# Optimization experiments

Hardware: AMD Instinct MI355X
Metric: run time of the kernel (lower is better)

## Reference

```python
import jax, jax.numpy as jnp
import numpy as np

N_NODES = 50000
N_EDGES = 1600000
POS_DIM = 64
IN_FEATS = 128
OUT_FEATS = 128
EDGE_MLP_DIM = 32


def setup_inputs() -> dict:
    key = jax.random.key(0)
    ks = jax.random.split(key, 8)
    x = jax.random.normal(ks[0], (N_NODES, POS_DIM + IN_FEATS), dtype=jnp.float32)
    edge_index = jax.random.randint(ks[1], (2, N_EDGES), 0, N_NODES, dtype=jnp.int32)
    # glorot for weight_noformer [in_feats, out_feats]
    stdv = float(np.sqrt(6.0 / (IN_FEATS + OUT_FEATS)))
    w_no = jax.random.uniform(ks[2], (IN_FEATS, OUT_FEATS), dtype=jnp.float32, minval=-stdv, maxval=stdv)
    bias = jnp.zeros((OUT_FEATS,), dtype=jnp.float32)
    # edge MLP: Linear(1, 32) -> Linear(32, 1) -> Sigmoid (no inner activation, faithful to source)
    lim1 = float(np.sqrt(1.0 / 1.0))
    mlp_w1 = jax.random.uniform(ks[3], (1, EDGE_MLP_DIM), dtype=jnp.float32, minval=-lim1, maxval=lim1)
    mlp_b1 = jax.random.uniform(ks[4], (EDGE_MLP_DIM,), dtype=jnp.float32, minval=-lim1, maxval=lim1)
    lim2 = float(np.sqrt(1.0 / EDGE_MLP_DIM))
    mlp_w2 = jax.random.uniform(ks[5], (EDGE_MLP_DIM, 1), dtype=jnp.float32, minval=-lim2, maxval=lim2)
    mlp_b2 = jax.random.uniform(ks[6], (1,), dtype=jnp.float32, minval=-lim2, maxval=lim2)
    return {"x": x, "edge_index": edge_index, "w_no": w_no, "bias": bias,
            "mlp_w1": mlp_w1, "mlp_b1": mlp_b1, "mlp_w2": mlp_w2, "mlp_b2": mlp_b2}


def reference(x, edge_index, w_no, bias, mlp_w1, mlp_b1, mlp_w2, mlp_b2):
    N = x.shape[0]
    coors = x[:, :POS_DIM]            # [N, pos_dim]
    feats = x[:, POS_DIM:]            # [N, in_feats]

    # gcn_norm with added self-loops (improved=False -> fill value 1)
    loop = jnp.arange(N, dtype=edge_index.dtype)
    row = jnp.concatenate([edge_index[0], loop])   # source
    col = jnp.concatenate([edge_index[1], loop])   # target
    ew = jnp.ones(row.shape[0], dtype=x.dtype)
    deg = jax.ops.segment_sum(ew, col, num_segments=N)
    dinv = jnp.where(deg > 0, jax.lax.rsqrt(deg), 0.0)
    ew = dinv[row] * ew * dinv[col]                # [E+N]

    # per-edge squared relative distance in positional space
    rel = coors[row] - coors[col]                  # [E+N, pos_dim]
    rel_dist = jnp.sum(rel * rel, axis=-1, keepdims=True)  # [E+N, 1]

    # tiny edge MLP + sigmoid (Linear -> Linear -> sigmoid)
    h = rel_dist @ mlp_w1 + mlp_b1                 # [E+N, mlp_dim]
    pe = jax.nn.sigmoid(h @ mlp_w2 + mlp_b2)       # [E+N, 1]

    # message = pe * norm_weight * x_j ; scatter-add into target nodes
    msg = pe * ew[:, None] * feats[row]            # [E+N, in_feats]
    m_i = jax.ops.segment_sum(msg, col, num_segments=N)  # [N, in_feats]

    hidden = m_i @ w_no + bias                     # [N, out_feats]
    return jnp.concatenate([coors, hidden], axis=-1)
```

## Files before the change

### kernel.cpp

```cpp
#include <hip/hip_runtime.h>
#include <math.h>

constexpr int NN = 50000;
constexpr int NE = 1600000;
constexpr int PD = 64;
constexpr int XD = 192;

constexpr int NB   = 3125;
constexpr int CAPF = 768;
constexpr int NCB  = 196;
constexpr int CAPC = 10240;
constexpr int RBLK = 782;
constexpr int CH2  = 5;

constexpr int OFF_NSQ   = 64;
constexpr int OFF_DINV  = OFF_NSQ   + 50048;
constexpr int OFF_HPRE  = OFF_DINV  + 50048;
constexpr int OFF_CCUR  = OFF_HPRE  + 50048;
constexpr int OFF_FCUR  = OFF_CCUR  + 256;
constexpr int OFF_CDATA = OFF_FCUR  + 3136;
constexpr int OFF_BDATA = OFF_CDATA + NCB * CAPC;
constexpr int OFF_CBQ   = OFF_BDATA + NB * CAPF;
constexpr int OFF_FBQ   = OFF_CBQ   + NN * 16;
constexpr int OFF_WBT   = OFF_FBQ   + NN * 32;

typedef __attribute__((ext_vector_type(8))) short bf16x8;
typedef __attribute__((ext_vector_type(4))) float f32x4;
typedef __attribute__((ext_vector_type(2))) float f32x2;

__device__ __forceinline__ unsigned short f2bf(float f) {
    unsigned u = __float_as_uint(f);
    return (unsigned short)((u + 0x7FFFu + ((u >> 16) & 1u)) >> 16);
}

__global__ __launch_bounds__(256) void k_pack(const float* __restrict__ x,
                                              const int* __restrict__ rowv,
                                              const int* __restrict__ colv,
                                              const float* __restrict__ w_no,
                                              const float* __restrict__ w1,
                                              const float* __restrict__ b1,
                                              const float* __restrict__ w2,
                                              const float* __restrict__ b2,
                                              float* __restrict__ out,
                                              unsigned* __restrict__ cbq,
                                              unsigned* __restrict__ fbqu,
                                              unsigned* __restrict__ ccur,
                                              unsigned* __restrict__ cdata,
                                              unsigned short* __restrict__ wbt,
                                              float* __restrict__ nsq,
                                              float* __restrict__ AB) {
    __shared__ int hist[NCB];
    __shared__ int pre[NCB];
    __shared__ unsigned gbase[NCB];
    __shared__ int scanbuf[256];
    __shared__ unsigned stag[2048];
    __shared__ unsigned char binof[2048];

    int t = threadIdx.x;
    if (blockIdx.x < RBLK) {
        int base = blockIdx.x * 2048;
        int cnt = NE - base; if (cnt > 2048) cnt = 2048;
        for (int i = t; i < NCB; i += 256) hist[i] = 0;
        __syncthreads();
        unsigned myrec[8]; int mybin[8], myrank[8];
        #pragma unroll
        for (int j = 0; j < 8; ++j) {
            int idx = base + j * 256 + t;
            mybin[j] = -1;
            if (idx < NE) {
                int c = colv[idx], r = rowv[idx];
                int bin = c >> 8;
                mybin[j]  = bin;
                myrank[j] = atomicAdd(&hist[bin], 1);
                myrec[j]  = ((unsigned)c << 16) | (unsigned)r;
            }
        }
        __syncthreads();
        int v = (t < NCB) ? hist[t] : 0;
        scanbuf[t] = v; __syncthreads();
        for (int d = 1; d < 256; d <<= 1) {
            int u = (t >= d) ? scanbuf[t - d] : 0;
            __syncthreads(); scanbuf[t] += u; __syncthreads();
        }
        if (t < NCB) {
            pre[t]   = scanbuf[t] - v;
            gbase[t] = v ? atomicAdd(&ccur[t], (unsigned)v) : 0u;
        }
        __syncthreads();
        #pragma unroll
        for (int j = 0; j < 8; ++j) {
            if (mybin[j] >= 0) {
                int slot = pre[mybin[j]] + myrank[j];
                stag[slot]  = myrec[j];
                binof[slot] = (unsigned char)mybin[j];
            }
        }
        __syncthreads();
        for (int s = t; s < cnt; s += 256) {
            int bin = binof[s];
            unsigned dst = gbase[bin] + (unsigned)(s - pre[bin]);
            if (dst < CAPC)
                cdata[(size_t)bin * CAPC + dst] = stag[s];
        }
        return;
    }

    int tid = (blockIdx.x - RBLK) * 256 + t;
    if (tid < 16384) wbt[tid] = f2bf(w_no[(tid & 127) * 128 + (tid >> 7)]);
    if (tid == 0) {
        float a = 0.f, b = 0.f;
        for (int k = 0; k < 32; ++k) { a += w1[k] * w2[k]; b += b1[k] * w2[k]; }
        AB[0] = a; AB[1] = b + b2[0];
    }
    int wid = tid >> 6, lane = tid & 63;
    if (wid < NN && lane < 48) {
        const float4 v = *(const float4*)&x[(size_t)wid * XD + lane * 4];
        if (lane < 16) {
            *(float4*)&out[(size_t)wid * XD + lane * 4] = v;
            unsigned p = 0;
            p = __builtin_amdgcn_cvt_pk_fp8_f32(v.x, v.y, p, false);
            p = __builtin_amdgcn_cvt_pk_fp8_f32(v.z, v.w, p, true);
            cbq[(size_t)wid * 16 + lane] = p;
            f32x2 lo = __builtin_amdgcn_cvt_pk_f32_fp8(p, false);
            f32x2 hi = __builtin_amdgcn_cvt_pk_f32_fp8(p, true);
            float ssq = lo.x * lo.x + lo.y * lo.y + hi.x * hi.x + hi.y * hi.y;
            #pragma unroll
            for (int o = 8; o >= 1; o >>= 1) ssq += __shfl_xor(ssq, o);
            if (lane == 0) nsq[wid] = ssq;
        } else {
            unsigned p = 0;
            p = __builtin_amdgcn_cvt_pk_fp8_f32(v.x, v.y, p, false);
            p = __builtin_amdgcn_cvt_pk_fp8_f32(v.z, v.w, p, true);
            fbqu[(size_t)wid * 32 + (lane - 16)] = p;
        }
    }
}

__global__ __launch_bounds__(256) void k_scat2(const unsigned* __restrict__ ccur,
                                               const unsigned* __restrict__ cdata,
                                               unsigned* __restrict__ fcur,
                                               unsigned* __restrict__ bdata) {
    __shared__ int hist[16];
    __shared__ int pre[16];
    __shared__ unsigned gbase[16];
    __shared__ unsigned stag[2048];
    __shared__ unsigned char binof[2048];

    int cb = blockIdx.x / CH2, k = blockIdx.x % CH2;
    int len = (int)ccur[cb]; if (len > CAPC) len = CAPC;
    int base = k * 2048;
    if (base >= len) return;
    int cnt = len - base; if (cnt > 2048) cnt = 2048;
    int t = threadIdx.x;
    if (t < 16) hist[t] = 0;
    __syncthreads();

    const unsigned* seg = cdata + (size_t)cb * CAPC + base;
    unsigned myrec[8]; int mybin[8], myrank[8];
    #pragma unroll
    for (int j = 0; j < 8; ++j) {
        int idx = j * 256 + t;
        mybin[j] = -1;
        if (idx < cnt) {
            unsigned rec = seg[idx];
            int c = (int)(rec >> 16);
            int bin = (c >> 4) & 15;
            mybin[j]  = bin;
            myrank[j] = atomicAdd(&hist[bin], 1);
            myrec[j]  = ((unsigned)(c & 15) << 16) | (rec & 0xFFFFu);
        }
    }
    __syncthreads();
    if (t == 0) {
        int run = 0;
        for (int i = 0; i < 16; ++i) { pre[i] = run; run += hist[i]; }
    }
    __syncthreads();
    if (t < 16)
        gbase[t] = hist[t] ? atomicAdd(&fcur[cb * 16 + t], (unsigned)hist[t]) : 0u;
    __syncthreads();
    #pragma unroll
    for (int j = 0; j < 8; ++j) {
        if (mybin[j] >= 0) {
            int slot = pre[mybin[j]] + myrank[j];
            stag[slot]  = myrec[j];
            binof[slot] = (unsigned char)mybin[j];
        }
    }
    __syncthreads();
    for (int s = t; s < cnt; s += 256) {
        int bin = binof[s];
        unsigned dst = gbase[bin] + (unsigned)(s - pre[bin]);
        if (dst < CAPF)
            bdata[(size_t)(cb * 16 + bin) * CAPF + dst] = stag[s];
    }
}

__global__ __launch_bounds__(256) void k_deg(const unsigned* __restrict__ fcur,
                                             const unsigned* __restrict__ bdata,
                                             unsigned* __restrict__ fbqu,
                                             float* __restrict__ dinv,
                                             unsigned* __restrict__ hpre) {
    __shared__ int hist[16];
    __shared__ int pre[16];
    __shared__ float sdv[16];
    int b = blockIdx.x, t = threadIdx.x;
    if (t < 16) hist[t] = 0;
    __syncthreads();

    int cnt = (int)fcur[b]; if (cnt > CAPF) cnt = CAPF;
    const unsigned* seg = bdata + (size_t)b * CAPF;
    for (int g = t; g < cnt; g += 256)
        atomicAdd(&hist[seg[g] >> 16], 1);
    __syncthreads();
    if (t == 0) {
        int run = 0;
        for (int i = 0; i < 16; ++i) { pre[i] = run; run += hist[i]; }
    }
    __syncthreads();
    if (t < 16) {
        int d = b * 16 + t;
        float dv = rsqrtf((float)hist[t] + 1.0f);
        sdv[t] = dv;
        dinv[d] = dv;
        hpre[d] = ((unsigned)pre[t] << 16) | (unsigned)hist[t];
    }
    __syncthreads();
    for (int i = t; i < 512; i += 256) {
        int d5 = i >> 5, q = i & 31;
        size_t idx = (size_t)(b * 16 + d5) * 32 + q;
        unsigned u = fbqu[idx];
        float dv = sdv[d5];
        f32x2 dv2 = {dv, dv};
        f32x2 lo = dv2 * __builtin_amdgcn_cvt_pk_f32_fp8(u, false);
        f32x2 hi = dv2 * __builtin_amdgcn_cvt_pk_f32_fp8(u, true);
        unsigned p = 0;
        p = __builtin_amdgcn_cvt_pk_fp8_f32(lo.x, lo.y, p, false);
        p = __builtin_amdgcn_cvt_pk_fp8_f32(hi.x, hi.y, p, true);
        fbqu[idx] = p;
    }
}

__global__ __launch_bounds__(256) void k_gather(const unsigned* __restrict__ fcur,
                                                const unsigned* __restrict__ bdata,
                                                const unsigned* __restrict__ cbq,
                                                const unsigned char* __restrict__ fbq,
                                                const float* __restrict__ nsq,
                                                const float* __restrict__ dinv,
                                                const unsigned* __restrict__ hpre,
                                                const float* __restrict__ AB,
                                                const float* __restrict__ bias,
                                                const unsigned short* __restrict__ wbt,
                                                float* __restrict__ out) {
    __shared__ unsigned srcL[CAPF + 64];
    __shared__ float    wgtL[CAPF + 64];
    __shared__ uint4    dcq[16][4];
    __shared__ unsigned mLu[16][68];
    __shared__ int preS[16];
    __shared__ int degS[16];
    __shared__ int curL[16];
    __shared__ float dvd[16];
    __shared__ float nsd[16];

    int b = blockIdx.x, t = threadIdx.x;

    if (t < 16) {
        int d = b * 16 + t;
        unsigned hp = hpre[d];
        preS[t] = (int)(hp >> 16);
        degS[t] = (int)(hp & 0xFFFFu);
        curL[t] = (int)(hp >> 16);
        dvd[t] = dinv[d];
        nsd[t] = nsq[d];
    }
    if (t < 64)
        dcq[t >> 2][t & 3] = ((const uint4*)(cbq + (size_t)(b * 16 + (t >> 2)) * 16))[t & 3];
    __syncthreads();

    float A = AB[0], Bc = AB[1];
    float sigB = __builtin_amdgcn_rcpf(1.0f + __expf(-Bc));

    int group = t >> 2, sub = t & 3;
    int cnt = (int)fcur[b]; if (cnt > CAPF) cnt = CAPF;
    const unsigned* seg = bdata + (size_t)b * CAPF;
    for (int base = 0; base < cnt; base += 64) {
        int g = base + group;
        bool valid = g < cnt;
        int gc = valid ? g : cnt - 1;
        unsigned rec = seg[gc];
        int d5 = rec >> 16;
        int s  = rec & 0xFFFF;
        float ns = nsq[s];
        uint4 sq = ((const uint4*)(cbq + (size_t)s * 16))[sub];
        uint4 dq = dcq[d5][sub];
        f32x2 dots = {0.f, 0.f};
        dots += __builtin_amdgcn_cvt_pk_f32_fp8(sq.x, false) *
                __builtin_amdgcn_cvt_pk_f32_fp8(dq.x, false);
        dots += __builtin_amdgcn_cvt_pk_f32_fp8(sq.x, true) *
                __builtin_amdgcn_cvt_pk_f32_fp8(dq.x, true);
        dots += __builtin_amdgcn_cvt_pk_f32_fp8(sq.y, false) *
                __builtin_amdgcn_cvt_pk_f32_fp8(dq.y, false);
        dots += __builtin_amdgcn_cvt_pk_f32_fp8(sq.y, true) *
                __builtin_amdgcn_cvt_pk_f32_fp8(dq.y, true);
        dots += __builtin_amdgcn_cvt_pk_f32_fp8(sq.z, false) *
                __builtin_amdgcn_cvt_pk_f32_fp8(dq.z, false);
        dots += __builtin_amdgcn_cvt_pk_f32_fp8(sq.z, true) *
                __builtin_amdgcn_cvt_pk_f32_fp8(dq.z, true);
        dots += __builtin_amdgcn_cvt_pk_f32_fp8(sq.w, false) *
                __builtin_amdgcn_cvt_pk_f32_fp8(dq.w, false);
        dots += __builtin_amdgcn_cvt_pk_f32_fp8(sq.w, true) *
                __builtin_amdgcn_cvt_pk_f32_fp8(dq.w, true);
        float sp = dots.x + dots.y;
        sp += __shfl_xor(sp, 1);
        sp += __shfl_xor(sp, 2);
        float ss = ns + nsd[d5] - 2.0f * sp;
        float w  = dvd[d5] *
                   __builtin_amdgcn_rcpf(1.0f + __expf(-(A * ss + Bc)));
        if (valid && sub == 0) {
            int slot = atomicAdd(&curL[d5], 1);
            srcL[slot] = (unsigned)s;
            wgtL[slot] = w;
        }
    }
    __syncthreads();

    int wl = t >> 6, lane = t & 63;
    int eslot = lane >> 4, dg = lane & 15;

    for (int i = 0; i < 4; ++i) {
        int d5 = wl * 4 + i;
        int d  = b * 16 + d5;

        int deg = degS[d5], s0 = preS[d5];
        float dv = dvd[d5];
        float w0 = (eslot == 0) ? dv * sigB : 0.f;
        f32x2 w02 = {w0, w0};
        uint2 fd = *(const uint2*)(fbq + (size_t)d * 128 + dg * 8);
        f32x2 a01 = w02 * __builtin_amdgcn_cvt_pk_f32_fp8(fd.x, false);
        f32x2 a23 = w02 * __builtin_amdgcn_cvt_pk_f32_fp8(fd.x, true);
        f32x2 a45 = w02 * __builtin_amdgcn_cvt_pk_f32_fp8(fd.y, false);
        f32x2 a67 = w02 * __builtin_amdgcn_cvt_pk_f32_fp8(fd.y, true);

        #pragma unroll 4
        for (int j = 0; j < deg; j += 4) {
            int jj = j + eslot;
            int e  = s0 + ((jj < deg) ? jj : 0);
            float w = (jj < deg) ? wgtL[e] : 0.f;
            int s = (int)srcL[e];
            f32x2 w2 = {w, w};
            uint2 f = *(const uint2*)(fbq + (size_t)s * 128 + dg * 8);
            a01 += w2 * __builtin_amdgcn_cvt_pk_f32_fp8(f.x, false);
            a23 += w2 * __builtin_amdgcn_cvt_pk_f32_fp8(f.x, true);
            a45 += w2 * __builtin_amdgcn_cvt_pk_f32_fp8(f.y, false);
            a67 += w2 * __builtin_amdgcn_cvt_pk_f32_fp8(f.y, true);
        }
        float a0 = a01.x, a1 = a01.y, a2 = a23.x, a3 = a23.y;
        float a4 = a45.x, a5 = a45.y, a6 = a67.x, a7 = a67.y;
        a0 += __shfl_xor(a0, 16); a0 += __shfl_xor(a0, 32);
        a1 += __shfl_xor(a1, 16); a1 += __shfl_xor(a1, 32);
        a2 += __shfl_xor(a2, 16); a2 += __shfl_xor(a2, 32);
        a3 += __shfl_xor(a3, 16); a3 += __shfl_xor(a3, 32);
        a4 += __shfl_xor(a4, 16); a4 += __shfl_xor(a4, 32);
        a5 += __shfl_xor(a5, 16); a5 += __shfl_xor(a5, 32);
        a6 += __shfl_xor(a6, 16); a6 += __shfl_xor(a6, 32);
        a7 += __shfl_xor(a7, 16); a7 += __shfl_xor(a7, 32);

        if (lane < 16) {
            uint4 o;
            o.x = (unsigned)f2bf(a0) | ((unsigned)f2bf(a1) << 16);
            o.y = (unsigned)f2bf(a2) | ((unsigned)f2bf(a3) << 16);
            o.z = (unsigned)f2bf(a4) | ((unsigned)f2bf(a5) << 16);
            o.w = (unsigned)f2bf(a6) | ((unsigned)f2bf(a7) << 16);
            *(uint4*)&mLu[d5][dg * 4] = o;
        }
    }
    __syncthreads();

    {
        int l15 = lane & 15, kg = lane >> 4;
        f32x4 acc[2];
        acc[0] = (f32x4){0.f, 0.f, 0.f, 0.f};
        acc[1] = (f32x4){0.f, 0.f, 0.f, 0.f};
        #pragma unroll
        for (int kk = 0; kk < 4; ++kk) {
            bf16x8 a = *(const bf16x8*)&mLu[l15][kk * 16 + kg * 4];
            #pragma unroll
            for (int nt = 0; nt < 2; ++nt) {
                int col = wl * 32 + nt * 16 + l15;
                bf16x8 bf = *(const bf16x8*)&wbt[(size_t)col * 128 + kk * 32 + kg * 8];
                acc[nt] = __builtin_amdgcn_mfma_f32_16x16x32_bf16(a, bf, acc[nt], 0, 0, 0);
            }
        }
        #pragma unroll
        for (int nt = 0; nt < 2; ++nt) {
            int col = wl * 32 + nt * 16 + l15;
            float bv = bias[col];
            #pragma unroll
            for (int q = 0; q < 4; ++q) {
                int row = kg * 4 + q;
                out[(size_t)(b * 16 + row) * XD + PD + col] = acc[nt][q] + bv;
            }
        }
    }
}

extern "C" void kernel_launch(void* const* d_in, const int* in_sizes, int n_in,
                              void* d_out, int out_size, void* d_ws, size_t ws_size,
                              hipStream_t stream) {
    const float* x    = (const float*)d_in[0];
    const int*   ei   = (const int*)d_in[1];
    const float* w_no = (const float*)d_in[2];
    const float* bias = (const float*)d_in[3];
    const float* w1   = (const float*)d_in[4];
    const float* b1   = (const float*)d_in[5];
    const float* w2   = (const float*)d_in[6];
    const float* b2   = (const float*)d_in[7];
    float* out = (float*)d_out;
    float* ws  = (float*)d_ws;

    float*          AB    = ws;
    float*          nsq   = ws + OFF_NSQ;
    float*          dinv  = ws + OFF_DINV;
    unsigned*       hpre  = (unsigned*)(ws + OFF_HPRE);
    unsigned*       ccur  = (unsigned*)(ws + OFF_CCUR);
    unsigned*       fcur  = (unsigned*)(ws + OFF_FCUR);
    unsigned*       cdata = (unsigned*)(ws + OFF_CDATA);
    unsigned*       bdata = (unsigned*)(ws + OFF_BDATA);
    unsigned*       cbq   = (unsigned*)(ws + OFF_CBQ);
    unsigned*       fbq   = (unsigned*)(ws + OFF_FBQ);
    unsigned short* wbt   = (unsigned short*)(ws + OFF_WBT);

    hipMemsetAsync(ccur, 0, (size_t)(256 + 3136) * sizeof(int), stream);

    k_pack<<<RBLK + 12500, 256, 0, stream>>>(x, ei, ei + NE, w_no, w1, b1, w2, b2,
                                             out, cbq, fbq, ccur, cdata, wbt, nsq, AB);
    k_scat2<<<NCB * CH2, 256, 0, stream>>>(ccur, cdata, fcur, bdata);
    k_deg<<<NB, 256, 0, stream>>>(fcur, bdata, fbq, dinv, hpre);

    k_gather<<<NB, 256, 0, stream>>>(fcur, bdata, cbq, (const unsigned char*)fbq,
                                     nsq, dinv, hpre, AB, bias, wbt, out);
}
```

Measured before the change: 115.0 us.

## Fold degree histogram into scatter pass and shrink degree kernel to per-node scan

The scatter kernel now also builds a 256-bin per-node degree histogram in shared memory and atomically adds it into a global degree array reused from the hpre buffer. The old degree kernel, which re-read every bucketed edge record to count degrees, becomes a small 196-block kernel that derives dinv, per-bucket prefix offsets and the fp8 feature scaling from those counts. This removes a full pass over the edge bucket data, at the cost of extra shared and global atomics in the scatter kernel and a widened memset. The gather loop also gets an unroll-by-2 hint.

After: 121.0 us. +5.2%, slower.

```diff
diff --git a/kernel.cpp b/kernel.cpp
--- a/kernel.cpp
+++ b/kernel.cpp
@@ -139,10 +139,12 @@
 __global__ __launch_bounds__(256) void k_scat2(const unsigned* __restrict__ ccur,
                                                const unsigned* __restrict__ cdata,
                                                unsigned* __restrict__ fcur,
-                                               unsigned* __restrict__ bdata) {
+                                               unsigned* __restrict__ bdata,
+                                               unsigned* __restrict__ deg) {
     __shared__ int hist[16];
     __shared__ int pre[16];
     __shared__ unsigned gbase[16];
+    __shared__ int hist256[256];
     __shared__ unsigned stag[2048];
     __shared__ unsigned char binof[2048];
 
@@ -153,6 +155,7 @@
     int cnt = len - base; if (cnt > 2048) cnt = 2048;
     int t = threadIdx.x;
     if (t < 16) hist[t] = 0;
+    hist256[t] = 0;
     __syncthreads();
 
     const unsigned* seg = cdata + (size_t)cb * CAPC + base;
@@ -167,6 +170,7 @@
             int bin = (c >> 4) & 15;
             mybin[j]  = bin;
             myrank[j] = atomicAdd(&hist[bin], 1);
+            atomicAdd(&hist256[c & 255], 1);
             myrec[j]  = ((unsigned)(c & 15) << 16) | (rec & 0xFFFFu);
         }
     }
@@ -178,6 +182,7 @@
     __syncthreads();
     if (t < 16)
         gbase[t] = hist[t] ? atomicAdd(&fcur[cb * 16 + t], (unsigned)hist[t]) : 0u;
+    if (hist256[t]) atomicAdd(&deg[cb * 256 + t], (unsigned)hist256[t]);
     __syncthreads();
     #pragma unroll
     for (int j = 0; j < 8; ++j) {
@@ -196,42 +201,31 @@
     }
 }
 
-__global__ __launch_bounds__(256) void k_deg(const unsigned* __restrict__ fcur,
-                                             const unsigned* __restrict__ bdata,
-                                             unsigned* __restrict__ fbqu,
-                                             float* __restrict__ dinv,
-                                             unsigned* __restrict__ hpre) {
-    __shared__ int hist[16];
-    __shared__ int pre[16];
-    __shared__ float sdv[16];
+__global__ __launch_bounds__(256) void k_dinv(unsigned* __restrict__ hpre,
+                                              float* __restrict__ dinv,
+                                              unsigned* __restrict__ fbqu) {
+    __shared__ int sdeg[256];
+    __shared__ float sdv[256];
     int b = blockIdx.x, t = threadIdx.x;
-    if (t < 16) hist[t] = 0;
-    __syncthreads();
-
-    int cnt = (int)fcur[b]; if (cnt > CAPF) cnt = CAPF;
-    const unsigned* seg = bdata + (size_t)b * CAPF;
-    for (int g = t; g < cnt; g += 256)
-        atomicAdd(&hist[seg[g] >> 16], 1);
-    __syncthreads();
-    if (t == 0) {
-        int run = 0;
-        for (int i = 0; i < 16; ++i) { pre[i] = run; run += hist[i]; }
-    }
-    __syncthreads();
-    if (t < 16) {
-        int d = b * 16 + t;
-        float dv = rsqrtf((float)hist[t] + 1.0f);
-        sdv[t] = dv;
+    int d = b * 256 + t;
+    int deg = (d < NN) ? (int)hpre[d] : 0;
+    sdeg[t] = deg;
+    float dv = rsqrtf((float)deg + 1.0f);
+    sdv[t] = dv;
+    __syncthreads();
+    int pre = 0, b0 = t & ~15;
+    for (int j = b0; j < t; ++j) pre += sdeg[j];
+    if (d < NN) {
         dinv[d] = dv;
-        hpre[d] = ((unsigned)pre[t] << 16) | (unsigned)hist[t];
-    }
-    __syncthreads();
-    for (int i = t; i < 512; i += 256) {
-        int d5 = i >> 5, q = i & 31;
-        size_t idx = (size_t)(b * 16 + d5) * 32 + q;
+        hpre[d] = ((unsigned)pre << 16) | (unsigned)deg;
+    }
+    int nodes = NN - b * 256; if (nodes > 256) nodes = 256;
+    for (int i = t; i < nodes * 32; i += 256) {
+        int n5 = i >> 5, q = i & 31;
+        size_t idx = (size_t)(b * 256 + n5) * 32 + q;
         unsigned u = fbqu[idx];
-        float dv = sdv[d5];
-        f32x2 dv2 = {dv, dv};
+        float dvx = sdv[n5];
+        f32x2 dv2 = {dvx, dvx};
         f32x2 lo = dv2 * __builtin_amdgcn_cvt_pk_f32_fp8(u, false);
         f32x2 hi = dv2 * __builtin_amdgcn_cvt_pk_f32_fp8(u, true);
         unsigned p = 0;
@@ -283,6 +277,7 @@
     int group = t >> 2, sub = t & 3;
     int cnt = (int)fcur[b]; if (cnt > CAPF) cnt = CAPF;
     const unsigned* seg = bdata + (size_t)b * CAPF;
+    #pragma unroll 2
     for (int base = 0; base < cnt; base += 64) {
         int g = base + group;
         bool valid = g < cnt;
@@ -430,12 +425,12 @@
     unsigned*       fbq   = (unsigned*)(ws + OFF_FBQ);
     unsigned short* wbt   = (unsigned short*)(ws + OFF_WBT);
 
-    hipMemsetAsync(ccur, 0, (size_t)(256 + 3136) * sizeof(int), stream);
+    hipMemsetAsync(hpre, 0, (size_t)(50048 + 256 + 3136) * sizeof(int), stream);
 
     k_pack<<<RBLK + 12500, 256, 0, stream>>>(x, ei, ei + NE, w_no, w1, b1, w2, b2,
                                              out, cbq, fbq, ccur, cdata, wbt, nsq, AB);
-    k_scat2<<<NCB * CH2, 256, 0, stream>>>(ccur, cdata, fcur, bdata);
-    k_deg<<<NB, 256, 0, stream>>>(fcur, bdata, fbq, dinv, hpre);
+    k_scat2<<<NCB * CH2, 256, 0, stream>>>(ccur, cdata, fcur, bdata, hpre);
+    k_dinv<<<NCB, 256, 0, stream>>>(hpre, dinv, fbq);
 
     k_gather<<<NB, 256, 0, stream>>>(fcur, bdata, cbq, (const unsigned char*)fbq,
                                      nsq, dinv, hpre, AB, bias, wbt, out);
```

## Split node packing across pack and scatter kernels, compute distance directly

Applied to the files above, without the earlier changes.

Node packing (copying coordinates to the output and fp8-quantizing coords and features) is divided between k_pack and k_scat2. The extra blocks appended to k_scat2 can overlap the memory-bound packing with the second scatter pass. The per-node squared-norm precompute and its loads are removed, and the gather computes the sum of squared differences directly rather than norms minus twice the dot product. This also drops the nsq buffer and the shuffle reduction, and adds an unroll hint on the edge loop. The distance arithmetic costs slightly more but avoids cancellation error in the norm expansion.

New measurement: 107.0 us. -7.0%, faster.

```diff
diff --git a/kernel.cpp b/kernel.cpp
--- a/kernel.cpp
+++ b/kernel.cpp
@@ -12,9 +12,13 @@
 constexpr int CAPC = 10240;
 constexpr int RBLK = 782;
 constexpr int CH2  = 5;
-
-constexpr int OFF_NSQ   = 64;
-constexpr int OFF_DINV  = OFF_NSQ   + 50048;
+constexpr int SBLK = NCB * CH2;
+
+constexpr int NPB1 = 4167;
+constexpr int NPB2 = 8333;
+constexpr int NBASE2 = 16668;
+
+constexpr int OFF_DINV  = 64;
 constexpr int OFF_HPRE  = OFF_DINV  + 50048;
 constexpr int OFF_CCUR  = OFF_HPRE  + 50048;
 constexpr int OFF_FCUR  = OFF_CCUR  + 256;
@@ -31,6 +35,24 @@
 __device__ __forceinline__ unsigned short f2bf(float f) {
     unsigned u = __float_as_uint(f);
     return (unsigned short)((u + 0x7FFFu + ((u >> 16) & 1u)) >> 16);
+}
+
+__device__ __forceinline__ void nodepack(int wid, int lane,
+                                         const float* __restrict__ x,
+                                         float* __restrict__ out,
+                                         unsigned* __restrict__ cbq,
+                                         unsigned* __restrict__ fbqu) {
+    if (wid >= NN || lane >= 48) return;
+    const float4 v = *(const float4*)&x[(size_t)wid * XD + lane * 4];
+    unsigned p = 0;
+    p = __builtin_amdgcn_cvt_pk_fp8_f32(v.x, v.y, p, false);
+    p = __builtin_amdgcn_cvt_pk_fp8_f32(v.z, v.w, p, true);
+    if (lane < 16) {
+        *(float4*)&out[(size_t)wid * XD + lane * 4] = v;
+        cbq[(size_t)wid * 16 + lane] = p;
+    } else {
+        fbqu[(size_t)wid * 32 + (lane - 16)] = p;
+    }
 }
 
 __global__ __launch_bounds__(256) void k_pack(const float* __restrict__ x,
@@ -47,7 +69,6 @@
                                               unsigned* __restrict__ ccur,
                                               unsigned* __restrict__ cdata,
                                               unsigned short* __restrict__ wbt,
-                                              float* __restrict__ nsq,
                                               float* __restrict__ AB) {
     __shared__ int hist[NCB];
     __shared__ int pre[NCB];
@@ -105,53 +126,43 @@
         return;
     }
 
-    int tid = (blockIdx.x - RBLK) * 256 + t;
+    int nb = blockIdx.x - RBLK;
+    int tid = nb * 256 + t;
     if (tid < 16384) wbt[tid] = f2bf(w_no[(tid & 127) * 128 + (tid >> 7)]);
     if (tid == 0) {
         float a = 0.f, b = 0.f;
         for (int k = 0; k < 32; ++k) { a += w1[k] * w2[k]; b += b1[k] * w2[k]; }
         AB[0] = a; AB[1] = b + b2[0];
     }
-    int wid = tid >> 6, lane = tid & 63;
-    if (wid < NN && lane < 48) {
-        const float4 v = *(const float4*)&x[(size_t)wid * XD + lane * 4];
-        if (lane < 16) {
-            *(float4*)&out[(size_t)wid * XD + lane * 4] = v;
-            unsigned p = 0;
-            p = __builtin_amdgcn_cvt_pk_fp8_f32(v.x, v.y, p, false);
-            p = __builtin_amdgcn_cvt_pk_fp8_f32(v.z, v.w, p, true);
-            cbq[(size_t)wid * 16 + lane] = p;
-            f32x2 lo = __builtin_amdgcn_cvt_pk_f32_fp8(p, false);
-            f32x2 hi = __builtin_amdgcn_cvt_pk_f32_fp8(p, true);
-            float ssq = lo.x * lo.x + lo.y * lo.y + hi.x * hi.x + hi.y * hi.y;
-            #pragma unroll
-            for (int o = 8; o >= 1; o >>= 1) ssq += __shfl_xor(ssq, o);
-            if (lane == 0) nsq[wid] = ssq;
-        } else {
-            unsigned p = 0;
-            p = __builtin_amdgcn_cvt_pk_fp8_f32(v.x, v.y, p, false);
-            p = __builtin_amdgcn_cvt_pk_fp8_f32(v.z, v.w, p, true);
-            fbqu[(size_t)wid * 32 + (lane - 16)] = p;
-        }
-    }
+    nodepack(nb * 4 + (t >> 6), t & 63, x, out, cbq, fbqu);
 }
 
 __global__ __launch_bounds__(256) void k_scat2(const unsigned* __restrict__ ccur,
                                                const unsigned* __restrict__ cdata,
                                                unsigned* __restrict__ fcur,
-                                               unsigned* __restrict__ bdata) {
+                                               unsigned* __restrict__ bdata,
+                                               const float* __restrict__ x,
+                                               float* __restrict__ out,
+                                               unsigned* __restrict__ cbq,
+                                               unsigned* __restrict__ fbqu) {
     __shared__ int hist[16];
     __shared__ int pre[16];
     __shared__ unsigned gbase[16];
     __shared__ unsigned stag[2048];
     __shared__ unsigned char binof[2048];
 
+    int t = threadIdx.x;
+    if (blockIdx.x >= SBLK) {
+        int nb = blockIdx.x - SBLK;
+        nodepack(NBASE2 + nb * 4 + (t >> 6), t & 63, x, out, cbq, fbqu);
+        return;
+    }
+
     int cb = blockIdx.x / CH2, k = blockIdx.x % CH2;
     int len = (int)ccur[cb]; if (len > CAPC) len = CAPC;
     int base = k * 2048;
     if (base >= len) return;
     int cnt = len - base; if (cnt > 2048) cnt = 2048;
-    int t = threadIdx.x;
     if (t < 16) hist[t] = 0;
     __syncthreads();
 
@@ -198,9 +209,9 @@
 
 __global__ __launch_bounds__(256) void k_deg(const unsigned* __restrict__ fcur,
                                              const unsigned* __restrict__ bdata,
-                                             unsigned* __restrict__ fbqu,
                                              float* __restrict__ dinv,
-                                             unsigned* __restrict__ hpre) {
+                                             unsigned* __restrict__ hpre,
+                                             unsigned* __restrict__ fbqu) {
     __shared__ int hist[16];
     __shared__ int pre[16];
     __shared__ float sdv[16];
@@ -245,7 +256,6 @@
                                                 const unsigned* __restrict__ bdata,
                                                 const unsigned* __restrict__ cbq,
                                                 const unsigned char* __restrict__ fbq,
-                                                const float* __restrict__ nsq,
                                                 const float* __restrict__ dinv,
                                                 const unsigned* __restrict__ hpre,
                                                 const float* __restrict__ AB,
@@ -260,7 +270,6 @@
     __shared__ int degS[16];
     __shared__ int curL[16];
     __shared__ float dvd[16];
-    __shared__ float nsd[16];
 
     int b = blockIdx.x, t = threadIdx.x;
 
@@ -271,7 +280,6 @@
         degS[t] = (int)(hp & 0xFFFFu);
         curL[t] = (int)(hp >> 16);
         dvd[t] = dinv[d];
-        nsd[t] = nsq[d];
     }
     if (t < 64)
         dcq[t >> 2][t & 3] = ((const uint4*)(cbq + (size_t)(b * 16 + (t >> 2)) * 16))[t & 3];
@@ -283,6 +291,7 @@
     int group = t >> 2, sub = t & 3;
     int cnt = (int)fcur[b]; if (cnt > CAPF) cnt = CAPF;
     const unsigned* seg = bdata + (size_t)b * CAPF;
+    #pragma unroll 2
     for (int base = 0; base < cnt; base += 64) {
         int g = base + group;
         bool valid = g < cnt;
@@ -290,32 +299,39 @@
         unsigned rec = seg[gc];
         int d5 = rec >> 16;
         int s  = rec & 0xFFFF;
-        float ns = nsq[s];
         uint4 sq = ((const uint4*)(cbq + (size_t)s * 16))[sub];
         uint4 dq = dcq[d5][sub];
-        f32x2 dots = {0.f, 0.f};
-        dots += __builtin_amdgcn_cvt_pk_f32_fp8(sq.x, false) *
-                __builtin_amdgcn_cvt_pk_f32_fp8(dq.x, false);
-        dots += __builtin_amdgcn_cvt_pk_f32_fp8(sq.x, true) *
-                __builtin_amdgcn_cvt_pk_f32_fp8(dq.x, true);
-        dots += __builtin_amdgcn_cvt_pk_f32_fp8(sq.y, false) *
-                __builtin_amdgcn_cvt_pk_f32_fp8(dq.y, false);
-        dots += __builtin_amdgcn_cvt_pk_f32_fp8(sq.y, true) *
-                __builtin_amdgcn_cvt_pk_f32_fp8(dq.y, true);
-        dots += __builtin_amdgcn_cvt_pk_f32_fp8(sq.z, false) *
-                __builtin_amdgcn_cvt_pk_f32_fp8(dq.z, false);
-        dots += __builtin_amdgcn_cvt_pk_f32_fp8(sq.z, true) *
-                __builtin_amdgcn_cvt_pk_f32_fp8(dq.z, true);
-        dots += __builtin_amdgcn_cvt_pk_f32_fp8(sq.w, false) *
-                __builtin_amdgcn_cvt_pk_f32_fp8(dq.w, false);
-        dots += __builtin_amdgcn_cvt_pk_f32_fp8(sq.w, true) *
-                __builtin_amdgcn_cvt_pk_f32_fp8(dq.w, true);
-        float sp = dots.x + dots.y;
+        f32x2 acc2 = {0.f, 0.f};
+        f32x2 dd;
+        dd = __builtin_amdgcn_cvt_pk_f32_fp8(sq.x, false) -
+             __builtin_amdgcn_cvt_pk_f32_fp8(dq.x, false);
+        acc2 += dd * dd;
+        dd = __builtin_amdgcn_cvt_pk_f32_fp8(sq.x, true) -
+             __builtin_amdgcn_cvt_pk_f32_fp8(dq.x, true);
+        acc2 += dd * dd;
+        dd = __builtin_amdgcn_cvt_pk_f32_fp8(sq.y, false) -
+             __builtin_amdgcn_cvt_pk_f32_fp8(dq.y, false);
+        acc2 += dd * dd;
+        dd = __builtin_amdgcn_cvt_pk_f32_fp8(sq.y, true) -
+             __builtin_amdgcn_cvt_pk_f32_fp8(dq.y, true);
+        acc2 += dd * dd;
+        dd = __builtin_amdgcn_cvt_pk_f32_fp8(sq.z, false) -
+             __builtin_amdgcn_cvt_pk_f32_fp8(dq.z, false);
+        acc2 += dd * dd;
+        dd = __builtin_amdgcn_cvt_pk_f32_fp8(sq.z, true) -
+             __builtin_amdgcn_cvt_pk_f32_fp8(dq.z, true);
+        acc2 += dd * dd;
+        dd = __builtin_amdgcn_cvt_pk_f32_fp8(sq.w, false) -
+             __builtin_amdgcn_cvt_pk_f32_fp8(dq.w, false);
+        acc2 += dd * dd;
+        dd = __builtin_amdgcn_cvt_pk_f32_fp8(sq.w, true) -
+             __builtin_amdgcn_cvt_pk_f32_fp8(dq.w, true);
+        acc2 += dd * dd;
+        float sp = acc2.x + acc2.y;
         sp += __shfl_xor(sp, 1);
         sp += __shfl_xor(sp, 2);
-        float ss = ns + nsd[d5] - 2.0f * sp;
-        float w  = dvd[d5] *
-                   __builtin_amdgcn_rcpf(1.0f + __expf(-(A * ss + Bc)));
+        float w = dvd[d5] *
+                  __builtin_amdgcn_rcpf(1.0f + __expf(-(A * sp + Bc)));
         if (valid && sub == 0) {
             int slot = atomicAdd(&curL[d5], 1);
             srcL[slot] = (unsigned)s;
@@ -419,7 +435,6 @@
     float* ws  = (float*)d_ws;
 
     float*          AB    = ws;
-    float*          nsq   = ws + OFF_NSQ;
     float*          dinv  = ws + OFF_DINV;
     unsigned*       hpre  = (unsigned*)(ws + OFF_HPRE);
     unsigned*       ccur  = (unsigned*)(ws + OFF_CCUR);
@@ -432,11 +447,12 @@
 
     hipMemsetAsync(ccur, 0, (size_t)(256 + 3136) * sizeof(int), stream);
 
-    k_pack<<<RBLK + 12500, 256, 0, stream>>>(x, ei, ei + NE, w_no, w1, b1, w2, b2,
-                                             out, cbq, fbq, ccur, cdata, wbt, nsq, AB);
-    k_scat2<<<NCB * CH2, 256, 0, stream>>>(ccur, cdata, fcur, bdata);
-    k_deg<<<NB, 256, 0, stream>>>(fcur, bdata, fbq, dinv, hpre);
+    k_pack<<<RBLK + NPB1, 256, 0, stream>>>(x, ei, ei + NE, w_no, w1, b1, w2, b2,
+                                            out, cbq, fbq, ccur, cdata, wbt, AB);
+    k_scat2<<<SBLK + NPB2, 256, 0, stream>>>(ccur, cdata, fcur, bdata,
+                                             x, out, cbq, fbq);
+    k_deg<<<NB, 256, 0, stream>>>(fcur, bdata, dinv, hpre, fbq);
 
     k_gather<<<NB, 256, 0, stream>>>(fcur, bdata, cbq, (const unsigned char*)fbq,
-                                     nsq, dinv, hpre, AB, bias, wbt, out);
-}
+                                     dinv, hpre, AB, bias, wbt, out);
+}
```
